# Performance work log

Hardware: AMD Instinct MI355X
Metric: run time of the kernel (lower is better)

The kernel has to match this reference:

```python
import jax, jax.numpy as jnp
import numpy as np

D = 16        # attention features
H = 8         # heads (head_dim = 2)
L = 8         # encoder layers
FF = 16       # dim_feedforward
K = 35        # conv kernel = stride
SEQ_IN = 3500 # input length -> 100 patches
EPS = 1e-5


def layer_norm(x, g, b):
    mu = jnp.mean(x, axis=-1, keepdims=True)
    var = jnp.mean((x - mu) ** 2, axis=-1, keepdims=True)
    return (x - mu) * jax.lax.rsqrt(var + EPS) * g + b


def setup_inputs() -> dict:
    key = jax.random.key(0)
    ks = jax.random.split(key, 24)
    B = 2048
    s = 0.1
    inp = {
        "x": jax.random.normal(ks[0], (B, SEQ_IN), dtype=jnp.float32),
        "conv_w": jax.random.normal(ks[1], (D, K), dtype=jnp.float32) * s,   # Conv1d(1->16,k=35)
        "conv_b": jax.random.normal(ks[2], (D,), dtype=jnp.float32) * s,
        "cls_emb": jax.random.normal(ks[3], (1, 1, D), dtype=jnp.float32),
        # stacked per-layer params [L, ...]
        "Wqkv": jax.random.normal(ks[4], (L, 3 * D, D), dtype=jnp.float32) * s,
        "bqkv": jnp.zeros((L, 3 * D), dtype=jnp.float32),
        "Wo": jax.random.normal(ks[5], (L, D, D), dtype=jnp.float32) * s,
        "bo": jnp.zeros((L, D), dtype=jnp.float32),
        "W1": jax.random.normal(ks[6], (L, FF, D), dtype=jnp.float32) * s,
        "b1": jnp.zeros((L, FF), dtype=jnp.float32),
        "W2": jax.random.normal(ks[7], (L, D, FF), dtype=jnp.float32) * s,
        "b2": jnp.zeros((L, D), dtype=jnp.float32),
        "ln1_g": jnp.ones((L, D), dtype=jnp.float32),
        "ln1_b": jnp.zeros((L, D), dtype=jnp.float32),
        "ln2_g": jnp.ones((L, D), dtype=jnp.float32),
        "ln2_b": jnp.zeros((L, D), dtype=jnp.float32),
        "lnf_g": jnp.ones((D,), dtype=jnp.float32),
        "lnf_b": jnp.zeros((D,), dtype=jnp.float32),
        "end_w": jax.random.normal(ks[8], (100, D), dtype=jnp.float32) * s,  # Conv1d(16->100,k=1)
        "end_b": jnp.zeros((100,), dtype=jnp.float32),
        "head_w": jax.random.normal(ks[9], (1, 100), dtype=jnp.float32) * s, # Linear(100->1)
        "head_b": jnp.zeros((1,), dtype=jnp.float32),
    }
    return inp


def _forward(x, conv_w, conv_b, cls_emb, Wqkv, bqkv, Wo, bo, W1, b1, W2, b2,
             ln1_g, ln1_b, ln2_g, ln2_b, lnf_g, lnf_b, end_w, end_b, head_w, head_b):
    B = x.shape[0]
    # patch embed: stride==kernel Conv1d == blocked matmul. [B,100,35] @ [35,16]
    patches = x.reshape(B, SEQ_IN // K, K)
    h = jnp.einsum("bpk,fk->bpf", patches, conv_w) + conv_b  # [B,100,16]
    h = jnp.concatenate([jnp.broadcast_to(cls_emb, (B, 1, D)), h], axis=1)  # [B,101,16]
    S = h.shape[1]
    scale = 1.0 / jnp.sqrt(jnp.asarray(D // H, dtype=h.dtype))

    def layer(hc, p):
        wqkv, bq, wo, bob, w1, b1l, w2, b2l, g1, be1, g2, be2 = p
        qkv = jnp.einsum("bsd,ed->bse", hc, wqkv) + bq      # [B,S,48]
        q, k, v = jnp.split(qkv, 3, axis=-1)
        q = q.reshape(B, S, H, D // H)
        k = k.reshape(B, S, H, D // H)
        v = v.reshape(B, S, H, D // H)
        scores = jnp.einsum("bshd,bthd->bhst", q, k) * scale  # [B,H,S,S]
        attn = jax.nn.softmax(scores, axis=-1)
        ctx = jnp.einsum("bhst,bthd->bshd", attn, v).reshape(B, S, D)
        attn_out = jnp.einsum("bsd,od->bso", ctx, wo) + bob
        hc = layer_norm(hc + attn_out, g1, be1)               # post-norm
        ff = jnp.einsum("bsd,fd->bsf", hc, w1) + b1l
        ff = jnp.einsum("bsf,df->bsd", jax.nn.relu(ff), w2) + b2l
        hc = layer_norm(hc + ff, g2, be2)
        return hc, None

    params = (Wqkv, bqkv, Wo, bo, W1, b1, W2, b2, ln1_g, ln1_b, ln2_g, ln2_b)
    h, _ = jax.lax.scan(layer, h, params)
    h = layer_norm(h, lnf_g, lnf_b)
    cls = h[:, 0, :]                                          # [B,16]
    latent = cls @ end_w.T + end_b                            # 1x1 conv == linear, [B,100]
    logits = latent @ head_w.T + head_b                       # [B,1]
    return jax.nn.sigmoid(logits)


def reference(x, conv_w, conv_b, cls_emb, Wqkv, bqkv, Wo, bo, W1, b1, W2, b2,
              ln1_g, ln1_b, ln2_g, ln2_b, lnf_g, lnf_b, end_w, end_b, head_w, head_b):
    return _forward(x, conv_w, conv_b, cls_emb, Wqkv, bqkv, Wo, bo, W1, b1, W2, b2,
                    ln1_g, ln1_b, ln2_g, ln2_b, lnf_g, lnf_b, end_w, end_b, head_w, head_b)
```

## Files before the change

kernel.cpp:

```cpp
#include <hip/hip_runtime.h>
#include <math.h>

#define DD   16
#define NH   8
#define NL   8
#define FFD  16
#define KK   35
#define SEQ  3500
#define NP   100
#define SS   101
#define NBATCH 2
#define NT   256
#define ROWB 64
#define BATB (SS * ROWB)
#define NWPAIR 6144

typedef __fp16 h2 __attribute__((ext_vector_type(2)));

__device__ __forceinline__ float fdot2(h2 a, h2 b, float c) {
#if __has_builtin(__builtin_amdgcn_fdot2)
  return __builtin_amdgcn_fdot2(a, b, c, false);
#else
  return c + (float)a.x * (float)b.x + (float)a.y * (float)b.y;
#endif
}
__device__ __forceinline__ float exp2_fast(float x) {
#if __has_builtin(__builtin_amdgcn_exp2f)
  return __builtin_amdgcn_exp2f(x);
#else
  return exp2f(x);
#endif
}
__device__ __forceinline__ float rcp_fast(float x) {
#if __has_builtin(__builtin_amdgcn_rcpf)
  return __builtin_amdgcn_rcpf(x);
#else
  return 1.0f / x;
#endif
}
__device__ __forceinline__ h2 pk_h2(float a, float b) {
#if __has_builtin(__builtin_amdgcn_cvt_pkrtz)
  return __builtin_amdgcn_cvt_pkrtz(a, b);
#else
  h2 r; r.x = (__fp16)a; r.y = (__fp16)b; return r;
#endif
}
__device__ __forceinline__ unsigned pk_u(float a, float b) {
  return __builtin_bit_cast(unsigned, pk_h2(a, b));
}
__device__ __forceinline__ h2 as_h2(unsigned u) {
  return __builtin_bit_cast(h2, u);
}

__device__ __forceinline__ void lnorm16(float* h, const float* __restrict__ g,
                                        const float* __restrict__ bb) {
  float mu = 0.f;
  #pragma unroll
  for (int d = 0; d < DD; ++d) mu += h[d];
  mu *= (1.f / DD);
  float var = 0.f;
  #pragma unroll
  for (int d = 0; d < DD; ++d) { float c = h[d] - mu; var += c * c; }
  var *= (1.f / DD);
  const float r = rsqrtf(var + 1e-5f);
  #pragma unroll
  for (int d = 0; d < DD; ++d) h[d] = (h[d] - mu) * r * g[d] + bb[d];
}

__device__ __forceinline__ float dot16(const h2* hv, const unsigned* __restrict__ w, float acc) {
  #pragma unroll
  for (int i = 0; i < 8; ++i) acc = fdot2(hv[i], as_h2(w[i]), acc);
  return acc;
}

__global__ __launch_bounds__(256)
void pack_weights(const float* __restrict__ Wqkv, const float* __restrict__ Wo,
                  const float* __restrict__ W1,   const float* __restrict__ W2,
                  unsigned* __restrict__ dst)
{
  const int i = blockIdx.x * 256 + threadIdx.x;
  if (i >= NWPAIR) return;
  float a, b;
  if (i < 3072)      { a = Wqkv[2*i];        b = Wqkv[2*i+1]; }
  else if (i < 4096) { int j = i - 3072; a = Wo[2*j]; b = Wo[2*j+1]; }
  else if (i < 5120) { int j = i - 4096; a = W1[2*j]; b = W1[2*j+1]; }
  else               { int j = i - 5120; a = W2[2*j]; b = W2[2*j+1]; }
  dst[i] = pk_u(a, b);
}

__global__ __launch_bounds__(NT)
void transformer_fwd_g(const float* __restrict__ x,
                       const float* __restrict__ conv_w,  const float* __restrict__ conv_b,
                       const float* __restrict__ cls_emb,
                       const float* __restrict__ bqkv,
                       const float* __restrict__ bo,
                       const float* __restrict__ b1,
                       const float* __restrict__ b2,
                       const float* __restrict__ ln1_g,   const float* __restrict__ ln1_b,
                       const float* __restrict__ ln2_g,   const float* __restrict__ ln2_b,
                       const float* __restrict__ lnf_g,   const float* __restrict__ lnf_b,
                       const float* __restrict__ end_w,   const float* __restrict__ end_b,
                       const float* __restrict__ head_w,  const float* __restrict__ head_b,
                       float* __restrict__ out, char* __restrict__ ws,
                       const unsigned* __restrict__ wpk, int B)
{
  __shared__ float s_cls[NBATCH][DD];
  __shared__ float s_lat[NBATCH][NP];

  const int tid = threadIdx.x;
  const int j   = tid / SS;
  const int r   = tid - j * SS;
  const int b   = blockIdx.x * NBATCH + j;
  const bool act = (tid < NBATCH * SS) && (b < B);

  const uint4* kvreg = (const uint4*)(ws + (size_t)b * BATB);
  uint4*       kvwr  = (uint4*)(ws + (size_t)b * BATB);

  float h[DD];
  if (act) {
    if (r == 0) {
      #pragma unroll
      for (int d = 0; d < DD; ++d) h[d] = cls_emb[d];
    } else {
      const float* xp = x + (size_t)b * SEQ + (r - 1) * KK;
      float xv[KK];
      #pragma unroll
      for (int k = 0; k < KK; ++k) xv[k] = xp[k];
      #pragma unroll
      for (int f = 0; f < DD; ++f) {
        float acc = conv_b[f];
        #pragma unroll
        for (int k = 0; k < KK; ++k) acc += xv[k] * conv_w[f * KK + k];
        h[f] = acc;
      }
    }
  }

  const float qs = 1.4426950408889634f * 0.70710678118654752f;

  for (int l = 0; l < NL; ++l) {
    const unsigned* wq16 = wpk + l * 384;
    const unsigned* wo16 = wpk + 3072 + l * 128;
    const unsigned* w116 = wpk + 4096 + l * 128;
    const unsigned* w216 = wpk + 5120 + l * 128;
    const float* bq  = bqkv + l * (3 * DD);
    const float* bol = bo   + l * DD;
    const float* b1l = b1   + l * FFD;
    const float* b2l = b2   + l * DD;
    const float* g1  = ln1_g + l * DD;  const float* be1 = ln1_b + l * DD;
    const float* g2  = ln2_g + l * DD;  const float* be2 = ln2_b + l * DD;

    __syncthreads();

    h2 q2[NH];
    if (act) {
      h2 hv[8];
      #pragma unroll
      for (int i = 0; i < 8; ++i) hv[i] = pk_h2(h[2*i], h[2*i+1]);

      #pragma unroll
      for (int hh = 0; hh < NH; ++hh) {
        const float a0 = dot16(hv, &wq16[(2*hh    ) * 8], bq[2*hh]);
        const float a1 = dot16(hv, &wq16[(2*hh + 1) * 8], bq[2*hh+1]);
        q2[hh] = pk_h2(a0 * qs, a1 * qs);
      }
      unsigned row[16];
      #pragma unroll
      for (int e = 0; e < 16; e += 2) {
        const float a0 = dot16(hv, &wq16[(DD + e    ) * 8], bq[DD + e]);
        const float a1 = dot16(hv, &wq16[(DD + e + 1) * 8], bq[DD + e + 1]);
        row[e >> 1] = pk_u(a0, a1);
      }
      #pragma unroll
      for (int e = 0; e < 16; e += 2) {
        const float a0 = dot16(hv, &wq16[(2*DD + e    ) * 8], bq[2*DD + e]);
        const float a1 = dot16(hv, &wq16[(2*DD + e + 1) * 8], bq[2*DD + e + 1]);
        row[8 + (e >> 1)] = pk_u(a0, a1);
      }
      uint4* dst = kvwr + (size_t)r * 4;
      dst[0] = make_uint4(row[0],  row[1],  row[2],  row[3]);
      dst[1] = make_uint4(row[4],  row[5],  row[6],  row[7]);
      dst[2] = make_uint4(row[8],  row[9],  row[10], row[11]);
      dst[3] = make_uint4(row[12], row[13], row[14], row[15]);
    }
    __syncthreads();

    if (act) {
      float lsum[NH], cxx[NH], cxy[NH];
      #pragma unroll
      for (int hh = 0; hh < NH; ++hh) { lsum[hh] = 0.f; cxx[hh] = 0.f; cxy[hh] = 0.f; }

      uint4 c0 = kvreg[0], c1 = kvreg[1], c2 = kvreg[2], c3 = kvreg[3];
      #pragma unroll 2
      for (int t = 0; t < SS; ++t) {
        const int tn = (t + 1 < SS) ? (t + 1) : t;
        const uint4* np = kvreg + 4 * tn;
        const uint4 n0 = np[0], n1 = np[1], n2 = np[2], n3 = np[3];

        const unsigned ku[8] = {c0.x, c0.y, c0.z, c0.w, c1.x, c1.y, c1.z, c1.w};
        const unsigned vu[8] = {c2.x, c2.y, c2.z, c2.w, c3.x, c3.y, c3.z, c3.w};
        #pragma unroll
        for (int hh = 0; hh < NH; ++hh) {
          const h2 kk = as_h2(ku[hh]);
          const h2 vv = as_h2(vu[hh]);
          const float p = exp2_fast(fdot2(q2[hh], kk, 0.0f));
          lsum[hh] += p;
          cxx[hh]  += (float)vv.x * p;
          cxy[hh]  += (float)vv.y * p;
        }
        c0 = n0; c1 = n1; c2 = n2; c3 = n3;
      }

      float cx[DD];
      #pragma unroll
      for (int hh = 0; hh < NH; ++hh) {
        const float inv = rcp_fast(lsum[hh]);
        cx[2 * hh]     = cxx[hh] * inv;
        cx[2 * hh + 1] = cxy[hh] * inv;
      }

      h2 cv[8];
      #pragma unroll
      for (int i = 0; i < 8; ++i) cv[i] = pk_h2(cx[2*i], cx[2*i+1]);
      #pragma unroll
      for (int od = 0; od < DD; ++od)
        h[od] += dot16(cv, &wo16[od * 8], bol[od]);
      lnorm16(h, g1, be1);

      h2 hv2[8];
      #pragma unroll
      for (int i = 0; i < 8; ++i) hv2[i] = pk_h2(h[2*i], h[2*i+1]);
      float fv[FFD];
      #pragma unroll
      for (int f = 0; f < FFD; ++f)
        fv[f] = fmaxf(dot16(hv2, &w116[f * 8], b1l[f]), 0.f);
      h2 fv2[8];
      #pragma unroll
      for (int i = 0; i < 8; ++i) fv2[i] = pk_h2(fv[2*i], fv[2*i+1]);
      #pragma unroll
      for (int od = 0; od < DD; ++od)
        h[od] += dot16(fv2, &w216[od * 8], b2l[od]);
      lnorm16(h, g2, be2);
    }
  }

  __syncthreads();
  if (act && r == 0) {
    lnorm16(h, lnf_g, lnf_b);
    #pragma unroll
    for (int d = 0; d < DD; ++d) s_cls[j][d] = h[d];
  }
  __syncthreads();
  if (tid < NBATCH * NP) {
    const int jj = tid / NP;
    const int oo = tid - jj * NP;
    if (blockIdx.x * NBATCH + jj < B) {
      float acc = end_b[oo];
      #pragma unroll
      for (int d = 0; d < DD; ++d) acc += s_cls[jj][d] * end_w[oo * DD + d];
      s_lat[jj][oo] = acc * head_w[oo];
    }
  }
  __syncthreads();
  if (tid < NBATCH) {
    const int bb = blockIdx.x * NBATCH + tid;
    if (bb < B) {
      float acc = head_b[0];
      for (int o = 0; o < NP; ++o) acc += s_lat[tid][o];
      out[bb] = rcp_fast(1.f + exp2_fast(-acc * 1.4426950408889634f));
    }
  }
}

#define FB_NBATCH 3
#define FB_NT 320
#define KROW 8
#define VROW 8
#define KREG (SS * KROW + 4)
#define VREG (SS * VROW + 2)
typedef float f2 __attribute__((ext_vector_type(2)));

__global__ __launch_bounds__(FB_NT)
void transformer_fwd_lds(const float* __restrict__ x,
                         const float* __restrict__ conv_w,  const float* __restrict__ conv_b,
                         const float* __restrict__ cls_emb,
                         const float* __restrict__ Wqkv,    const float* __restrict__ bqkv,
                         const float* __restrict__ Wo,      const float* __restrict__ bo,
                         const float* __restrict__ W1,      const float* __restrict__ b1,
                         const float* __restrict__ W2,      const float* __restrict__ b2,
                         const float* __restrict__ ln1_g,   const float* __restrict__ ln1_b,
                         const float* __restrict__ ln2_g,   const float* __restrict__ ln2_b,
                         const float* __restrict__ lnf_g,   const float* __restrict__ lnf_b,
                         const float* __restrict__ end_w,   const float* __restrict__ end_b,
                         const float* __restrict__ head_w,  const float* __restrict__ head_b,
                         float* __restrict__ out, int B)
{
  __shared__ h2    s_K[FB_NBATCH][KREG];
  __shared__ f2    s_V[FB_NBATCH][VREG];
  __shared__ float s_cls[FB_NBATCH][DD];
  __shared__ float s_lat[FB_NBATCH][NP];

  const int tid = threadIdx.x;
  const int j   = tid / SS;
  const int r   = tid - j * SS;
  const int b   = blockIdx.x * FB_NBATCH + j;
  const bool act = (tid < FB_NBATCH * SS) && (b < B);

  float h[DD];
  if (act) {
    if (r == 0) {
      #pragma unroll
      for (int d = 0; d < DD; ++d) h[d] = cls_emb[d];
    } else {
      const float* xp = x + (size_t)b * SEQ + (r - 1) * KK;
      float xv[KK];
      #pragma unroll
      for (int k = 0; k < KK; ++k) xv[k] = xp[k];
      #pragma unroll
      for (int f = 0; f < DD; ++f) {
        float acc = conv_b[f];
        #pragma unroll
        for (int k = 0; k < KK; ++k) acc += xv[k] * conv_w[f * KK + k];
        h[f] = acc;
      }
    }
  }

  const float qs = 1.4426950408889634f * 0.70710678118654752f;

  for (int l = 0; l < NL; ++l) {
    const float* wq  = Wqkv + l * (3 * DD * DD);
    const float* bq  = bqkv + l * (3 * DD);
    const float* wo  = Wo   + l * (DD * DD);
    const float* bol = bo   + l * DD;
    const float* w1  = W1   + l * (FFD * DD);
    const float* b1l = b1   + l * FFD;
    const float* w2  = W2   + l * (DD * FFD);
    const float* b2l = b2   + l * DD;
    const float* g1  = ln1_g + l * DD;  const float* be1 = ln1_b + l * DD;
    const float* g2  = ln2_g + l * DD;  const float* be2 = ln2_b + l * DD;

    __syncthreads();

    h2 q2[NH];
    if (act) {
      #pragma unroll
      for (int hh = 0; hh < NH; ++hh) {
        const int e0 = 2 * hh;
        float a0 = bq[e0], a1 = bq[e0 + 1];
        #pragma unroll
        for (int d = 0; d < DD; ++d) {
          a0 += h[d] * wq[e0 * DD + d];
          a1 += h[d] * wq[(e0 + 1) * DD + d];
        }
        q2[hh] = pk_h2(a0 * qs, a1 * qs);
      }
      h2* kw = &s_K[j][r * KROW];
      #pragma unroll
      for (int hh = 0; hh < NH; ++hh) {
        const int e0 = DD + 2 * hh;
        float a0 = bq[e0], a1 = bq[e0 + 1];
        #pragma unroll
        for (int d = 0; d < DD; ++d) {
          a0 += h[d] * wq[e0 * DD + d];
          a1 += h[d] * wq[(e0 + 1) * DD + d];
        }
        kw[hh] = pk_h2(a0, a1);
      }
      f2* vw = &s_V[j][r * VROW];
      #pragma unroll
      for (int hh = 0; hh < NH; ++hh) {
        const int e0 = 2 * DD + 2 * hh;
        float a0 = bq[e0], a1 = bq[e0 + 1];
        #pragma unroll
        for (int d = 0; d < DD; ++d) {
          a0 += h[d] * wq[e0 * DD + d];
          a1 += h[d] * wq[(e0 + 1) * DD + d];
        }
        f2 vv; vv.x = a0; vv.y = a1;
        vw[hh] = vv;
      }
    }
    __syncthreads();

    if (act) {
      float lsum[NH];
      f2 ctx[NH];
      #pragma unroll
      for (int hh = 0; hh < NH; ++hh) { lsum[hh] = 0.f; ctx[hh].x = 0.f; ctx[hh].y = 0.f; }
      const h2* kp0 = &s_K[j][0];
      const f2* vp0 = &s_V[j][0];
      for (int t = 0; t < SS; ++t) {
        const h2* kp = kp0 + t * KROW;
        const f2* vp = vp0 + t * VROW;
        #pragma unroll
        for (int hh = 0; hh < NH; ++hh) {
          const float p = exp2_fast(fdot2(q2[hh], kp[hh], 0.0f));
          lsum[hh] += p;
          ctx[hh]  += vp[hh] * p;
        }
      }
      float cx[DD];
      #pragma unroll
      for (int hh = 0; hh < NH; ++hh) {
        const float inv = rcp_fast(lsum[hh]);
        cx[2 * hh]     = ctx[hh].x * inv;
        cx[2 * hh + 1] = ctx[hh].y * inv;
      }
      #pragma unroll
      for (int od = 0; od < DD; ++od) {
        float acc = bol[od];
        #pragma unroll
        for (int d = 0; d < DD; ++d) acc += cx[d] * wo[od * DD + d];
        h[od] += acc;
      }
      lnorm16(h, g1, be1);
      float fv[FFD];
      #pragma unroll
      for (int f = 0; f < FFD; ++f) {
        float acc = b1l[f];
        #pragma unroll
        for (int d = 0; d < DD; ++d) acc += h[d] * w1[f * DD + d];
        fv[f] = fmaxf(acc, 0.f);
      }
      #pragma unroll
      for (int od = 0; od < DD; ++od) {
        float acc = b2l[od];
        #pragma unroll
        for (int f = 0; f < FFD; ++f) acc += fv[f] * w2[od * FFD + f];
        h[od] += acc;
      }
      lnorm16(h, g2, be2);
    }
  }

  __syncthreads();
  if (act && r == 0) {
    lnorm16(h, lnf_g, lnf_b);
    #pragma unroll
    for (int d = 0; d < DD; ++d) s_cls[j][d] = h[d];
  }
  __syncthreads();
  if (tid < FB_NBATCH * NP) {
    const int jj = tid / NP;
    const int oo = tid - jj * NP;
    if (blockIdx.x * FB_NBATCH + jj < B) {
      float acc = end_b[oo];
      #pragma unroll
      for (int d = 0; d < DD; ++d) acc += s_cls[jj][d] * end_w[oo * DD + d];
      s_lat[jj][oo] = acc * head_w[oo];
    }
  }
  __syncthreads();
  if (tid < FB_NBATCH) {
    const int bb = blockIdx.x * FB_NBATCH + tid;
    if (bb < B) {
      float acc = head_b[0];
      for (int o = 0; o < NP; ++o) acc += s_lat[tid][o];
      out[bb] = rcp_fast(1.f + exp2_fast(-acc * 1.4426950408889634f));
    }
  }
}

extern "C" void kernel_launch(void* const* d_in, const int* in_sizes, int n_in,
                              void* d_out, int out_size, void* d_ws, size_t ws_size,
                              hipStream_t stream) {
  const float* x       = (const float*)d_in[0];
  const float* conv_w  = (const float*)d_in[1];
  const float* conv_b  = (const float*)d_in[2];
  const float* cls_emb = (const float*)d_in[3];
  const float* Wqkv    = (const float*)d_in[4];
  const float* bqkv    = (const float*)d_in[5];
  const float* Wo      = (const float*)d_in[6];
  const float* bo      = (const float*)d_in[7];
  const float* W1      = (const float*)d_in[8];
  const float* b1      = (const float*)d_in[9];
  const float* W2      = (const float*)d_in[10];
  const float* b2      = (const float*)d_in[11];
  const float* ln1_g   = (const float*)d_in[12];
  const float* ln1_b   = (const float*)d_in[13];
  const float* ln2_g   = (const float*)d_in[14];
  const float* ln2_b   = (const float*)d_in[15];
  const float* lnf_g   = (const float*)d_in[16];
  const float* lnf_b   = (const float*)d_in[17];
  const float* end_w   = (const float*)d_in[18];
  const float* end_b   = (const float*)d_in[19];
  const float* head_w  = (const float*)d_in[20];
  const float* head_b  = (const float*)d_in[21];
  float* out = (float*)d_out;

  const int B = in_sizes[0] / SEQ;
  const size_t kv_bytes = (size_t)B * BATB;
  const size_t need     = kv_bytes + NWPAIR * sizeof(unsigned);

  if (ws_size >= need) {
    unsigned* wpk = (unsigned*)((char*)d_ws + kv_bytes);
    pack_weights<<<(NWPAIR + 255) / 256, 256, 0, stream>>>(Wqkv, Wo, W1, W2, wpk);
    const int nb = (B + NBATCH - 1) / NBATCH;
    transformer_fwd_g<<<nb, NT, 0, stream>>>(
        x, conv_w, conv_b, cls_emb, bqkv, bo, b1, b2,
        ln1_g, ln1_b, ln2_g, ln2_b, lnf_g, lnf_b, end_w, end_b, head_w, head_b,
        out, (char*)d_ws, wpk, B);
  } else {
    const int nb = (B + FB_NBATCH - 1) / FB_NBATCH;
    transformer_fwd_lds<<<nb, FB_NT, 0, stream>>>(
        x, conv_w, conv_b, cls_emb, Wqkv, bqkv, Wo, bo, W1, b1, W2, b2,
        ln1_g, ln1_b, ln2_g, ln2_b, lnf_g, lnf_b, end_w, end_b, head_w, head_b,
        out, B);
  }
}
```

Before: 590.1 us.

## Stage per-layer K/V rows in shared memory instead of global workspace

Moves the per-token packed K/V rows from a global workspace buffer into an LDS array with a padded 20-dword row stride, so the attention loop reads them from shared memory rather than L2/HBM. Threads are remapped so each sequence uses two full wavefronts (128 lanes, 101 active). Launch bounds now request 4 blocks per CU. The LDS footprint (about 16KB per block) and the register cap implied by the occupancy hint may limit residency or cause spills, and the padded rows and idle lanes waste some capacity.

```diff
diff --git a/kernel.cpp b/kernel.cpp
--- a/kernel.cpp
+++ b/kernel.cpp
@@ -11,8 +11,8 @@
 #define SS   101
 #define NBATCH 2
 #define NT   256
-#define ROWB 64
-#define BATB (SS * ROWB)
+#define ROWDW 20
+#define NROW 102
 #define NWPAIR 6144
 
 typedef __fp16 h2 __attribute__((ext_vector_type(2)));
@@ -88,7 +88,7 @@
   dst[i] = pk_u(a, b);
 }
 
-__global__ __launch_bounds__(NT)
+__global__ __launch_bounds__(NT, 4)
 void transformer_fwd_g(const float* __restrict__ x,
                        const float* __restrict__ conv_w,  const float* __restrict__ conv_b,
                        const float* __restrict__ cls_emb,
@@ -101,20 +101,20 @@
                        const float* __restrict__ lnf_g,   const float* __restrict__ lnf_b,
                        const float* __restrict__ end_w,   const float* __restrict__ end_b,
                        const float* __restrict__ head_w,  const float* __restrict__ head_b,
-                       float* __restrict__ out, char* __restrict__ ws,
+                       float* __restrict__ out,
                        const unsigned* __restrict__ wpk, int B)
 {
+  __shared__ unsigned s_kv[NBATCH][NROW * ROWDW];
   __shared__ float s_cls[NBATCH][DD];
   __shared__ float s_lat[NBATCH][NP];
 
-  const int tid = threadIdx.x;
-  const int j   = tid / SS;
-  const int r   = tid - j * SS;
-  const int b   = blockIdx.x * NBATCH + j;
-  const bool act = (tid < NBATCH * SS) && (b < B);
-
-  const uint4* kvreg = (const uint4*)(ws + (size_t)b * BATB);
-  uint4*       kvwr  = (uint4*)(ws + (size_t)b * BATB);
+  const int tid  = threadIdx.x;
+  const int wid  = tid >> 6;
+  const int lane = tid & 63;
+  const int j    = wid >> 1;
+  const int r    = ((wid & 1) << 6) + lane;
+  const int b    = blockIdx.x * NBATCH + j;
+  const bool act = (r < SS) && (b < B);
 
   float h[DD];
   if (act) {
@@ -177,7 +177,7 @@
         const float a1 = dot16(hv, &wq16[(2*DD + e + 1) * 8], bq[2*DD + e + 1]);
         row[8 + (e >> 1)] = pk_u(a0, a1);
       }
-      uint4* dst = kvwr + (size_t)r * 4;
+      uint4* dst = (uint4*)&s_kv[j][r * ROWDW];
       dst[0] = make_uint4(row[0],  row[1],  row[2],  row[3]);
       dst[1] = make_uint4(row[4],  row[5],  row[6],  row[7]);
       dst[2] = make_uint4(row[8],  row[9],  row[10], row[11]);
@@ -190,11 +190,11 @@
       #pragma unroll
       for (int hh = 0; hh < NH; ++hh) { lsum[hh] = 0.f; cxx[hh] = 0.f; cxy[hh] = 0.f; }
 
-      uint4 c0 = kvreg[0], c1 = kvreg[1], c2 = kvreg[2], c3 = kvreg[3];
+      const uint4* kv = (const uint4*)&s_kv[j][0];
+      uint4 c0 = kv[0], c1 = kv[1], c2 = kv[2], c3 = kv[3];
       #pragma unroll 2
       for (int t = 0; t < SS; ++t) {
-        const int tn = (t + 1 < SS) ? (t + 1) : t;
-        const uint4* np = kvreg + 4 * tn;
+        const uint4* np = kv + 5 * (t + 1);
         const uint4 n0 = np[0], n1 = np[1], n2 = np[2], n3 = np[3];
 
         const unsigned ku[8] = {c0.x, c0.y, c0.z, c0.w, c1.x, c1.y, c1.z, c1.w};
@@ -490,17 +490,15 @@
   float* out = (float*)d_out;
 
   const int B = in_sizes[0] / SEQ;
-  const size_t kv_bytes = (size_t)B * BATB;
-  const size_t need     = kv_bytes + NWPAIR * sizeof(unsigned);
-
-  if (ws_size >= need) {
-    unsigned* wpk = (unsigned*)((char*)d_ws + kv_bytes);
+
+  if (ws_size >= NWPAIR * sizeof(unsigned)) {
+    unsigned* wpk = (unsigned*)d_ws;
     pack_weights<<<(NWPAIR + 255) / 256, 256, 0, stream>>>(Wqkv, Wo, W1, W2, wpk);
     const int nb = (B + NBATCH - 1) / NBATCH;
     transformer_fwd_g<<<nb, NT, 0, stream>>>(
         x, conv_w, conv_b, cls_emb, bqkv, bo, b1, b2,
         ln1_g, ln1_b, ln2_g, ln2_b, lnf_g, lnf_b, end_w, end_b, head_w, head_b,
-        out, (char*)d_ws, wpk, B);
+        out, wpk, B);
   } else {
     const int nb = (B + FB_NBATCH - 1) / FB_NBATCH;
     transformer_fwd_lds<<<nb, FB_NT, 0, stream>>>(
```

Measured after the change: 590.1 us. About the same (-0.0%).
